# Optimization experiments

Hardware: AMD Instinct MI355X
Metric: run time of the kernel (lower is better)

The kernel has to match this reference:

```python
import jax, jax.numpy as jnp
import numpy as np

NQ = 4          # n_qubits -> 2**4 = 16 amplitudes
NL = 3          # n_layers
TWO_PI = 2.0 * np.pi
BN_EPS = 1e-5


def _ry_batched(t):
    # t: [B] -> [B,2,2] complex64
    c, s = jnp.cos(t / 2), jnp.sin(t / 2)
    g = jnp.stack([jnp.stack([c, -s], -1), jnp.stack([s, c], -1)], -2)
    return g.astype(jnp.complex64)


def _ry(t):
    c, s = jnp.cos(t / 2), jnp.sin(t / 2)
    return jnp.stack([jnp.stack([c, -s]), jnp.stack([s, c])]).astype(jnp.complex64)


def _rz(t):
    e = jnp.stack([jnp.exp(-0.5j * t), jnp.exp(0.5j * t)]).astype(jnp.complex64)
    return jnp.diag(e)


def _apply_1q(state, gate, wire, batched):
    # state: [B,2,2,2,2]; gate: [2,2] or [B,2,2]
    s = jnp.moveaxis(state, wire + 1, -1)
    if batched:
        s = jnp.einsum('bij,b...j->b...i', gate, s)
    else:
        s = jnp.einsum('ij,...j->...i', gate, s)
    return jnp.moveaxis(s, -1, wire + 1)


def _apply_cnot(state, c, t):
    s = jnp.moveaxis(state, (c + 1, t + 1), (-2, -1))
    s = jnp.stack([s[..., 0, :], s[..., 1, ::-1]], axis=-2)  # flip target when control=1
    return jnp.moveaxis(s, (-2, -1), (c + 1, t + 1))


def _circuit(angles, weights):
    # angles: [B, NQ] float32; weights: [NL, NQ, 2]
    B = angles.shape[0]
    state = jnp.zeros((B,) + (2,) * NQ, jnp.complex64)
    state = state.at[(slice(None),) + (0,) * NQ].set(1.0)
    # input encoding RYs (per-sample angles -> batched gates)
    for i in range(NQ):
        state = _apply_1q(state, _ry_batched(angles[:, i]), i, True)
    for layer in range(NL):
        for i in range(NQ):
            state = _apply_1q(state, _ry(weights[layer, i, 0]), i, False)
            state = _apply_1q(state, _rz(weights[layer, i, 1]), i, False)
        for i in range(NQ - 1):
            state = _apply_cnot(state, i, i + 1)
        state = _apply_cnot(state, NQ - 1, 0)
    probs = jnp.abs(state) ** 2  # [B,2,2,2,2] real
    zs = []
    for i in range(NQ):
        axes = tuple(a for a in range(1, NQ + 1) if a != i + 1)
        pm = probs.sum(axis=axes)  # [B,2]
        zs.append(pm[:, 0] - pm[:, 1])
    return jnp.stack(zs, -1).astype(jnp.float32)  # [B,NQ]


def setup_inputs() -> dict:
    key = jax.random.key(0)
    ks = jax.random.split(key, 4)
    B = 524288
    x = jax.random.normal(ks[0], (B, 16), jnp.float32)
    weights = jax.random.normal(ks[1], (NL, NQ, 2), jnp.float32)
    fc_w = jax.random.normal(ks[2], (4, NQ), jnp.float32) / np.sqrt(NQ)
    fc_b = jax.random.normal(ks[3], (4,), jnp.float32) * 0.01
    gamma = jnp.ones((4,), jnp.float32)
    beta = jnp.zeros((4,), jnp.float32)
    return {"x": x, "weights": weights, "fc_w": fc_w, "fc_b": fc_b,
            "gamma": gamma, "beta": beta}


def reference(x, weights, fc_w, fc_b, gamma, beta):
    inp = x.reshape(x.shape[0], -1)[:, :NQ]
    mn, mx = inp.min(), inp.max()  # global min/max as in the torch code
    angles = TWO_PI * (inp - mn) / (mx - mn + 1e-8)
    q = _circuit(angles, weights)                # [B,4] PauliZ expvals
    out = q @ fc_w.T + fc_b                      # Linear(4,4)
    mean = out.mean(0)
    var = out.var(0)                             # biased, as torch BN training
    return gamma * (out - mean) / jnp.sqrt(var + BN_EPS) + beta
```

## Files before the change

### kernel.cpp

```cpp
#include <hip/hip_runtime.h>
#include <math.h>

#define TWO_PI_F 6.28318530717958647692f
#define BN_EPS_F 1e-5f

#define MINK_OFF 0
#define MAXK_OFF 16
#define STAT_OFF 32
#define STAT_STRIDE 32
#define A_OFF 288
#define UR_OFF 384
#define UI_OFF 640

__device__ __forceinline__ unsigned f2key(float f) {
  unsigned u = __float_as_uint(f);
  return (u & 0x80000000u) ? ~u : (u | 0x80000000u);
}
__device__ __forceinline__ float key2f(unsigned k) {
  unsigned u = (k & 0x80000000u) ? (k ^ 0x80000000u) : ~k;
  return __uint_as_float(u);
}

__global__ void k_init(const float* __restrict__ w, const float* __restrict__ fc_w,
                       float* __restrict__ wsf) {
  int t = threadIdx.x;
  if (t == 0) {
    unsigned* wsu = (unsigned*)wsf;
    wsu[MINK_OFF] = 0xFFFFFFFFu;
    wsu[MAXK_OFF] = 0x00000000u;
#pragma unroll
    for (int j = 0; j < 8; ++j) wsf[STAT_OFF + j * STAT_STRIDE] = 0.0f;
    for (int j = 0; j < 4; ++j)
      for (int k = 0; k < 16; ++k) {
        float s = 0.f;
        for (int i = 0; i < 4; ++i)
          s += fc_w[j * 4 + i] * ((k & (8 >> i)) ? -1.f : 1.f);
        wsf[A_OFF + j * 16 + k] = s;
      }
  }
  if (t < 16) {
    float sr[16], si[16];
#pragma unroll
    for (int k = 0; k < 16; ++k) { sr[k] = (k == t) ? 1.f : 0.f; si[k] = 0.f; }
#pragma unroll
    for (int l = 0; l < 3; ++l) {
#pragma unroll
      for (int i = 0; i < 4; ++i) {
        const int m = 8 >> i;
        float ryc, rys, rzc, rzs;
        __sincosf(0.5f * w[(l * 4 + i) * 2 + 0], &rys, &ryc);
        __sincosf(0.5f * w[(l * 4 + i) * 2 + 1], &rzs, &rzc);
#pragma unroll
        for (int k = 0; k < 16; ++k) {
          if (!(k & m)) {
            int k1 = k | m;
            float a0r = sr[k], a0i = si[k], a1r = sr[k1], a1i = si[k1];
            sr[k]  = ryc * a0r - rys * a1r;
            si[k]  = ryc * a0i - rys * a1i;
            sr[k1] = rys * a0r + ryc * a1r;
            si[k1] = rys * a0i + ryc * a1i;
          }
        }
#pragma unroll
        for (int k = 0; k < 16; ++k) {
          float ps = (k & m) ? rzs : -rzs;
          float r = sr[k], ii = si[k];
          sr[k] = r * rzc - ii * ps;
          si[k] = r * ps + ii * rzc;
        }
      }
#pragma unroll
      for (int c = 0; c < 4; ++c) {
        const int mc = 8 >> c;
        const int mt = 8 >> ((c + 1) & 3);
#pragma unroll
        for (int k = 0; k < 16; ++k) {
          if ((k & mc) && !(k & mt)) {
            int k2 = k | mt;
            float tt;
            tt = sr[k]; sr[k] = sr[k2]; sr[k2] = tt;
            tt = si[k]; si[k] = si[k2]; si[k2] = tt;
          }
        }
      }
    }
#pragma unroll
    for (int k = 0; k < 16; ++k) {
      wsf[UR_OFF + k * 16 + t] = sr[k];
      wsf[UI_OFF + k * 16 + t] = si[k];
    }
  }
}

__global__ __launch_bounds__(256) void k_minmax(const float* __restrict__ x,
                                                unsigned* __restrict__ wsu, int B) {
  float fmn = __builtin_inff();
  float fmx = -__builtin_inff();
  for (int r = blockIdx.x * blockDim.x + threadIdx.x; r < B;
       r += gridDim.x * blockDim.x) {
    float4 v = *(const float4*)(x + (size_t)r * 16);
    fmn = fminf(fmn, fminf(fminf(v.x, v.y), fminf(v.z, v.w)));
    fmx = fmaxf(fmx, fmaxf(fmaxf(v.x, v.y), fmaxf(v.z, v.w)));
  }
#pragma unroll
  for (int d = 32; d; d >>= 1) {
    fmn = fminf(fmn, __shfl_down(fmn, d));
    fmx = fmaxf(fmx, __shfl_down(fmx, d));
  }
  __shared__ float smn[4], smx[4];
  int wave = threadIdx.x >> 6, lane = threadIdx.x & 63;
  if (lane == 0) { smn[wave] = fmn; smx[wave] = fmx; }
  __syncthreads();
  if (threadIdx.x == 0) {
    float bmn = fminf(fminf(smn[0], smn[1]), fminf(smn[2], smn[3]));
    float bmx = fmaxf(fmaxf(smx[0], smx[1]), fmaxf(smx[2], smx[3]));
    atomicMin(&wsu[MINK_OFF], f2key(bmn));
    atomicMax(&wsu[MAXK_OFF], f2key(bmx));
  }
}

__global__ __launch_bounds__(256) void k_main(const float* __restrict__ x,
                                              const float* __restrict__ wsf,
                                              const float* __restrict__ fc_b,
                                              float* __restrict__ out, int B) {
  int b = blockIdx.x * 256 + threadIdx.x;
  const unsigned* wsu = (const unsigned*)wsf;
  float mn = key2f(wsu[MINK_OFF]);
  float mx = key2f(wsu[MAXK_OFF]);
  float denom = mx - mn + 1e-8f;

  float o[4] = {0.f, 0.f, 0.f, 0.f};
  if (b < B) {
    float4 xv = *(const float4*)(x + (size_t)b * 16);
    float ang[4] = {TWO_PI_F * (xv.x - mn) / denom, TWO_PI_F * (xv.y - mn) / denom,
                    TWO_PI_F * (xv.z - mn) / denom, TWO_PI_F * (xv.w - mn) / denom};
    float cq[4], sq[4];
#pragma unroll
    for (int i = 0; i < 4; ++i) __sincosf(0.5f * ang[i], &sq[i], &cq[i]);

    float v[16];
#pragma unroll
    for (int k = 0; k < 16; ++k) {
      v[k] = ((k & 8) ? sq[0] : cq[0]) * ((k & 4) ? sq[1] : cq[1]) *
             ((k & 2) ? sq[2] : cq[2]) * ((k & 1) ? sq[3] : cq[3]);
    }

    const float* __restrict__ Ur = wsf + UR_OFF;
    const float* __restrict__ Ui = wsf + UI_OFF;
    float yr[16], yi[16];
#pragma unroll
    for (int k = 0; k < 16; ++k) { yr[k] = 0.f; yi[k] = 0.f; }
#pragma unroll
    for (int a = 0; a < 16; ++a) {
      float va = v[a];
#pragma unroll
      for (int k = 0; k < 16; ++k) {
        yr[k] = fmaf(Ur[k * 16 + a], va, yr[k]);
        yi[k] = fmaf(Ui[k * 16 + a], va, yi[k]);
      }
    }

    const float* __restrict__ A = wsf + A_OFF;
    o[0] = fc_b[0]; o[1] = fc_b[1]; o[2] = fc_b[2]; o[3] = fc_b[3];
#pragma unroll
    for (int k = 0; k < 16; ++k) {
      float p = yr[k] * yr[k] + yi[k] * yi[k];
      o[0] = fmaf(A[0 * 16 + k], p, o[0]);
      o[1] = fmaf(A[1 * 16 + k], p, o[1]);
      o[2] = fmaf(A[2 * 16 + k], p, o[2]);
      o[3] = fmaf(A[3 * 16 + k], p, o[3]);
    }
    *(float4*)(out + (size_t)b * 4) = make_float4(o[0], o[1], o[2], o[3]);
  }

  float vals[8] = {o[0], o[1], o[2], o[3],
                   o[0] * o[0], o[1] * o[1], o[2] * o[2], o[3] * o[3]};
#pragma unroll
  for (int j = 0; j < 8; ++j) {
#pragma unroll
    for (int d = 32; d; d >>= 1) vals[j] += __shfl_down(vals[j], d);
  }
  __shared__ float red[4][8];
  int wave = threadIdx.x >> 6, lane = threadIdx.x & 63;
  if (lane == 0) {
#pragma unroll
    for (int j = 0; j < 8; ++j) red[wave][j] = vals[j];
  }
  __syncthreads();
  if (threadIdx.x < 8) {
    float s = red[0][threadIdx.x] + red[1][threadIdx.x] + red[2][threadIdx.x] +
              red[3][threadIdx.x];
    atomicAdd((float*)wsf + STAT_OFF + threadIdx.x * STAT_STRIDE, s);
  }
}

__global__ __launch_bounds__(256) void k_final(float* __restrict__ out,
                                               const float* __restrict__ wsf,
                                               const float* __restrict__ gamma,
                                               const float* __restrict__ beta, int B) {
  int b = blockIdx.x * 256 + threadIdx.x;
  if (b >= B) return;
  float inv = 1.0f / (float)B;
  float4 v = *(float4*)(out + (size_t)b * 4);
  float vv[4] = {v.x, v.y, v.z, v.w};
  float res[4];
#pragma unroll
  for (int j = 0; j < 4; ++j) {
    float mean = wsf[STAT_OFF + j * STAT_STRIDE] * inv;
    float var = wsf[STAT_OFF + (4 + j) * STAT_STRIDE] * inv - mean * mean;
    res[j] = gamma[j] * (vv[j] - mean) * rsqrtf(var + BN_EPS_F) + beta[j];
  }
  *(float4*)(out + (size_t)b * 4) = make_float4(res[0], res[1], res[2], res[3]);
}

extern "C" void kernel_launch(void* const* d_in, const int* in_sizes, int n_in,
                              void* d_out, int out_size, void* d_ws, size_t ws_size,
                              hipStream_t stream) {
  const float* x     = (const float*)d_in[0];
  const float* w     = (const float*)d_in[1];
  const float* fc_w  = (const float*)d_in[2];
  const float* fc_b  = (const float*)d_in[3];
  const float* gamma = (const float*)d_in[4];
  const float* beta  = (const float*)d_in[5];
  float* out = (float*)d_out;
  float* wsf = (float*)d_ws;
  unsigned* wsu = (unsigned*)d_ws;
  int B = in_sizes[0] / 16;

  k_init<<<1, 64, 0, stream>>>(w, fc_w, wsf);
  k_minmax<<<1024, 256, 0, stream>>>(x, wsu, B);
  k_main<<<(B + 255) / 256, 256, 0, stream>>>(x, wsf, fc_b, out, B);
  k_final<<<(B + 255) / 256, 256, 0, stream>>>(out, wsf, gamma, beta, B);
}
```

Measured before the change: 137.6 us.

## Fuse minmax, circuit, and batchnorm into one cooperative grid-synced kernel

Replaces the four-kernel pipeline with a single cooperative kernel. Each thread loads its four samples once and keeps them in registers across two grid syncs: one for the global min/max, one for the batch-norm statistics. This removes the separate min/max pass over the input, the write and re-read of the intermediate output, and several launches. It also processes two samples per inner loop to reuse table loads and drops the bias, which cancels under batch norm. It relies on every block being co-resident, and it keeps a multi-kernel fallback if the cooperative launch fails.

```diff
diff --git a/kernel.cpp b/kernel.cpp
--- a/kernel.cpp
+++ b/kernel.cpp
@@ -1,16 +1,21 @@
 #include <hip/hip_runtime.h>
+#include <hip/hip_cooperative_groups.h>
 #include <math.h>
+
+namespace cg = cooperative_groups;
 
 #define TWO_PI_F 6.28318530717958647692f
 #define BN_EPS_F 1e-5f
-
-#define MINK_OFF 0
-#define MAXK_OFF 16
-#define STAT_OFF 32
+#define NBC 512
+#define NT 256
+
+#define STAT_OFF 0
 #define STAT_STRIDE 32
-#define A_OFF 288
-#define UR_OFF 384
-#define UI_OFF 640
+#define BMIN_OFF 256
+#define BMAX_OFF 768
+#define TAB_OFF 1280
+#define MINK_OFF 1856
+#define MAXK_OFF 1888
 
 __device__ __forceinline__ unsigned f2key(float f) {
   unsigned u = __float_as_uint(f);
@@ -21,27 +26,13 @@
   return __uint_as_float(u);
 }
 
-__global__ void k_init(const float* __restrict__ w, const float* __restrict__ fc_w,
-                       float* __restrict__ wsf) {
-  int t = threadIdx.x;
-  if (t == 0) {
-    unsigned* wsu = (unsigned*)wsf;
-    wsu[MINK_OFF] = 0xFFFFFFFFu;
-    wsu[MAXK_OFF] = 0x00000000u;
-#pragma unroll
-    for (int j = 0; j < 8; ++j) wsf[STAT_OFF + j * STAT_STRIDE] = 0.0f;
-    for (int j = 0; j < 4; ++j)
-      for (int k = 0; k < 16; ++k) {
-        float s = 0.f;
-        for (int i = 0; i < 4; ++i)
-          s += fc_w[j * 4 + i] * ((k & (8 >> i)) ? -1.f : 1.f);
-        wsf[A_OFF + j * 16 + k] = s;
-      }
-  }
-  if (t < 16) {
+__device__ void build_tables(int tid, const float* __restrict__ w,
+                             const float* __restrict__ fc_w, float* wsf,
+                             bool init_keys) {
+  if (tid < 16) {
     float sr[16], si[16];
 #pragma unroll
-    for (int k = 0; k < 16; ++k) { sr[k] = (k == t) ? 1.f : 0.f; si[k] = 0.f; }
+    for (int k = 0; k < 16; ++k) { sr[k] = (k == tid) ? 1.f : 0.f; si[k] = 0.f; }
 #pragma unroll
     for (int l = 0; l < 3; ++l) {
 #pragma unroll
@@ -55,8 +46,8 @@
           if (!(k & m)) {
             int k1 = k | m;
             float a0r = sr[k], a0i = si[k], a1r = sr[k1], a1i = si[k1];
-            sr[k]  = ryc * a0r - rys * a1r;
-            si[k]  = ryc * a0i - rys * a1i;
+            sr[k] = ryc * a0r - rys * a1r;
+            si[k] = ryc * a0i - rys * a1i;
             sr[k1] = rys * a0r + ryc * a1r;
             si[k1] = rys * a0i + ryc * a1i;
           }
@@ -86,16 +77,208 @@
     }
 #pragma unroll
     for (int k = 0; k < 16; ++k) {
-      wsf[UR_OFF + k * 16 + t] = sr[k];
-      wsf[UI_OFF + k * 16 + t] = si[k];
-    }
-  }
-}
-
-__global__ __launch_bounds__(256) void k_minmax(const float* __restrict__ x,
-                                                unsigned* __restrict__ wsu, int B) {
-  float fmn = __builtin_inff();
-  float fmx = -__builtin_inff();
+      wsf[TAB_OFF + tid * 16 + k] = sr[k];
+      wsf[TAB_OFF + 256 + tid * 16 + k] = si[k];
+    }
+  } else if (tid == 16) {
+    for (int k = 0; k < 16; ++k)
+      for (int j = 0; j < 4; ++j) {
+        float s = 0.f;
+        for (int i = 0; i < 4; ++i)
+          s += fc_w[j * 4 + i] * ((k & (8 >> i)) ? -1.f : 1.f);
+        wsf[TAB_OFF + 512 + k * 4 + j] = s;
+      }
+  } else if (tid == 17 && init_keys) {
+    unsigned* wsu = (unsigned*)wsf;
+    wsu[MINK_OFF] = 0xFFFFFFFFu;
+    wsu[MAXK_OFF] = 0x00000000u;
+  } else if (tid >= 24 && tid < 32) {
+    wsf[STAT_OFF + (tid - 24) * STAT_STRIDE] = 0.0f;
+  }
+}
+
+template <int PAIR>
+__device__ __forceinline__ void qfc_pair(const float* __restrict__ tab,
+                                         const float* c0, const float* s0,
+                                         const float* c1, const float* s1,
+                                         float* o0, float* o1) {
+  const float* __restrict__ Ur = tab;
+  const float* __restrict__ Ui = tab + 256;
+  const float* __restrict__ At = tab + 512;
+  float A01_0[4] = {c0[0] * c0[1], c0[0] * s0[1], s0[0] * c0[1], s0[0] * s0[1]};
+  float A23_0[4] = {c0[2] * c0[3], c0[2] * s0[3], s0[2] * c0[3], s0[2] * s0[3]};
+  float A01_1[4] = {c1[0] * c1[1], c1[0] * s1[1], s1[0] * c1[1], s1[0] * s1[1]};
+  float A23_1[4] = {c1[2] * c1[3], c1[2] * s1[3], s1[2] * c1[3], s1[2] * s1[3]};
+  float yr0[16], yi0[16], yr1[16], yi1[16];
+#pragma unroll
+  for (int k = 0; k < 16; ++k) { yr0[k] = yi0[k] = yr1[k] = yi1[k] = 0.f; }
+#pragma unroll
+  for (int a = 0; a < 16; ++a) {
+    float va0 = A01_0[a >> 2] * A23_0[a & 3];
+    float va1 = A01_1[a >> 2] * A23_1[a & 3];
+#pragma unroll
+    for (int k = 0; k < 16; ++k) {
+      float ur = Ur[a * 16 + k], ui = Ui[a * 16 + k];
+      yr0[k] = fmaf(ur, va0, yr0[k]);
+      yi0[k] = fmaf(ui, va0, yi0[k]);
+      yr1[k] = fmaf(ur, va1, yr1[k]);
+      yi1[k] = fmaf(ui, va1, yi1[k]);
+    }
+  }
+#pragma unroll
+  for (int j = 0; j < 4; ++j) { o0[j] = 0.f; o1[j] = 0.f; }
+#pragma unroll
+  for (int k = 0; k < 16; ++k) {
+    float p0 = fmaf(yr0[k], yr0[k], yi0[k] * yi0[k]);
+    float p1 = fmaf(yr1[k], yr1[k], yi1[k] * yi1[k]);
+#pragma unroll
+    for (int j = 0; j < 4; ++j) {
+      float av = At[k * 4 + j];
+      o0[j] = fmaf(av, p0, o0[j]);
+      o1[j] = fmaf(av, p1, o1[j]);
+    }
+  }
+}
+
+__global__ __launch_bounds__(NT, 2) void k_fused(
+    const float* __restrict__ x, const float* __restrict__ w,
+    const float* __restrict__ fc_w, const float* __restrict__ gamma,
+    const float* __restrict__ beta, float* wsf,
+    const float* __restrict__ tab, float* __restrict__ out, int B) {
+  cg::grid_group grid = cg::this_grid();
+  const int tid = threadIdx.x;
+  const int gtid = blockIdx.x * NT + tid;
+  const int H = NBC * NT;
+  const int wv = tid >> 6, ln = tid & 63;
+  __shared__ float sred[4][8];
+
+  float4 xs[4];
+  bool hp[4];
+#pragma unroll
+  for (int p = 0; p < 4; ++p) {
+    int s = gtid + p * H;
+    hp[p] = s < B;
+    xs[p] = hp[p] ? *(const float4*)(x + (size_t)s * 16) : make_float4(0, 0, 0, 0);
+  }
+  float fmn = __builtin_inff(), fmx = -__builtin_inff();
+#pragma unroll
+  for (int p = 0; p < 4; ++p) {
+    if (hp[p]) {
+      fmn = fminf(fmn, fminf(fminf(xs[p].x, xs[p].y), fminf(xs[p].z, xs[p].w)));
+      fmx = fmaxf(fmx, fmaxf(fmaxf(xs[p].x, xs[p].y), fmaxf(xs[p].z, xs[p].w)));
+    }
+  }
+#pragma unroll
+  for (int d = 32; d; d >>= 1) {
+    fmn = fminf(fmn, __shfl_down(fmn, d));
+    fmx = fmaxf(fmx, __shfl_down(fmx, d));
+  }
+  if (ln == 0) { sred[wv][0] = fmn; sred[wv][1] = fmx; }
+  __syncthreads();
+  if (tid == 0) {
+    wsf[BMIN_OFF + blockIdx.x] =
+        fminf(fminf(sred[0][0], sred[1][0]), fminf(sred[2][0], sred[3][0]));
+    wsf[BMAX_OFF + blockIdx.x] =
+        fmaxf(fmaxf(sred[0][1], sred[1][1]), fmaxf(sred[2][1], sred[3][1]));
+  }
+  if (blockIdx.x == 0) build_tables(tid, w, fc_w, wsf, false);
+
+  __threadfence();
+  grid.sync();
+
+  float gm = __builtin_inff(), gM = -__builtin_inff();
+#pragma unroll
+  for (int q = 0; q < NBC / 64; ++q) {
+    int i = ln + q * 64;
+    gm = fminf(gm, wsf[BMIN_OFF + i]);
+    gM = fmaxf(gM, wsf[BMAX_OFF + i]);
+  }
+#pragma unroll
+  for (int d = 32; d; d >>= 1) {
+    gm = fminf(gm, __shfl_down(gm, d));
+    gM = fmaxf(gM, __shfl_down(gM, d));
+  }
+  gm = __shfl(gm, 0);
+  gM = __shfl(gM, 0);
+  const float ssc = TWO_PI_F * 0.5f / (gM - gm + 1e-8f);
+
+  float o[4][4];
+#pragma unroll
+  for (int pp = 0; pp < 2; ++pp) {
+    const float4 xa = xs[pp * 2], xb = xs[pp * 2 + 1];
+    float a0[4] = {xa.x, xa.y, xa.z, xa.w};
+    float a1[4] = {xb.x, xb.y, xb.z, xb.w};
+    float c0[4], s0[4], c1[4], s1[4];
+#pragma unroll
+    for (int i = 0; i < 4; ++i) {
+      __sincosf((a0[i] - gm) * ssc, &s0[i], &c0[i]);
+      __sincosf((a1[i] - gm) * ssc, &s1[i], &c1[i]);
+    }
+    qfc_pair<0>(tab, c0, s0, c1, s1, o[pp * 2], o[pp * 2 + 1]);
+  }
+
+  float vals[8];
+#pragma unroll
+  for (int j = 0; j < 4; ++j) {
+    float s = 0.f, ss = 0.f;
+#pragma unroll
+    for (int p = 0; p < 4; ++p) {
+      float v = hp[p] ? o[p][j] : 0.f;
+      s += v;
+      ss = fmaf(v, v, ss);
+    }
+    vals[j] = s;
+    vals[4 + j] = ss;
+  }
+#pragma unroll
+  for (int j = 0; j < 8; ++j) {
+#pragma unroll
+    for (int d = 32; d; d >>= 1) vals[j] += __shfl_down(vals[j], d);
+  }
+  __syncthreads();
+  if (ln == 0) {
+#pragma unroll
+    for (int j = 0; j < 8; ++j) sred[wv][j] = vals[j];
+  }
+  __syncthreads();
+  if (tid < 8) {
+    float s = sred[0][tid] + sred[1][tid] + sred[2][tid] + sred[3][tid];
+    atomicAdd(wsf + STAT_OFF + tid * STAT_STRIDE, s);
+  }
+
+  __threadfence();
+  grid.sync();
+
+  const float inv = 1.0f / (float)B;
+  float sc[4], sh[4];
+#pragma unroll
+  for (int j = 0; j < 4; ++j) {
+    float mean = wsf[STAT_OFF + j * STAT_STRIDE] * inv;
+    float var = wsf[STAT_OFF + (4 + j) * STAT_STRIDE] * inv - mean * mean;
+    float is = rsqrtf(var + BN_EPS_F);
+    sc[j] = gamma[j] * is;
+    sh[j] = beta[j] - mean * sc[j];
+  }
+#pragma unroll
+  for (int p = 0; p < 4; ++p) {
+    if (hp[p]) {
+      int s = gtid + p * H;
+      *(float4*)(out + (size_t)s * 4) =
+          make_float4(fmaf(o[p][0], sc[0], sh[0]), fmaf(o[p][1], sc[1], sh[1]),
+                      fmaf(o[p][2], sc[2], sh[2]), fmaf(o[p][3], sc[3], sh[3]));
+    }
+  }
+}
+
+__global__ void k_init_fb(const float* __restrict__ w,
+                          const float* __restrict__ fc_w, float* wsf) {
+  build_tables(threadIdx.x, w, fc_w, wsf, true);
+}
+
+__global__ __launch_bounds__(256) void k_minmax_fb(const float* __restrict__ x,
+                                                   unsigned* __restrict__ wsu,
+                                                   int B) {
+  float fmn = __builtin_inff(), fmx = -__builtin_inff();
   for (int r = blockIdx.x * blockDim.x + threadIdx.x; r < B;
        r += gridDim.x * blockDim.x) {
     float4 v = *(const float4*)(x + (size_t)r * 16);
@@ -108,96 +291,62 @@
     fmx = fmaxf(fmx, __shfl_down(fmx, d));
   }
   __shared__ float smn[4], smx[4];
-  int wave = threadIdx.x >> 6, lane = threadIdx.x & 63;
-  if (lane == 0) { smn[wave] = fmn; smx[wave] = fmx; }
+  int wv = threadIdx.x >> 6, ln = threadIdx.x & 63;
+  if (ln == 0) { smn[wv] = fmn; smx[wv] = fmx; }
   __syncthreads();
   if (threadIdx.x == 0) {
-    float bmn = fminf(fminf(smn[0], smn[1]), fminf(smn[2], smn[3]));
-    float bmx = fmaxf(fmaxf(smx[0], smx[1]), fmaxf(smx[2], smx[3]));
-    atomicMin(&wsu[MINK_OFF], f2key(bmn));
-    atomicMax(&wsu[MAXK_OFF], f2key(bmx));
-  }
-}
-
-__global__ __launch_bounds__(256) void k_main(const float* __restrict__ x,
-                                              const float* __restrict__ wsf,
-                                              const float* __restrict__ fc_b,
-                                              float* __restrict__ out, int B) {
+    atomicMin(&wsu[MINK_OFF],
+              f2key(fminf(fminf(smn[0], smn[1]), fminf(smn[2], smn[3]))));
+    atomicMax(&wsu[MAXK_OFF],
+              f2key(fmaxf(fmaxf(smx[0], smx[1]), fmaxf(smx[2], smx[3]))));
+  }
+}
+
+__global__ __launch_bounds__(256) void k_main_fb(const float* __restrict__ x,
+                                                 float* wsf,
+                                                 const float* __restrict__ tab,
+                                                 float* __restrict__ out, int B) {
   int b = blockIdx.x * 256 + threadIdx.x;
   const unsigned* wsu = (const unsigned*)wsf;
   float mn = key2f(wsu[MINK_OFF]);
   float mx = key2f(wsu[MAXK_OFF]);
-  float denom = mx - mn + 1e-8f;
-
-  float o[4] = {0.f, 0.f, 0.f, 0.f};
+  const float ssc = TWO_PI_F * 0.5f / (mx - mn + 1e-8f);
+  float o0[4] = {0, 0, 0, 0}, o1[4];
   if (b < B) {
     float4 xv = *(const float4*)(x + (size_t)b * 16);
-    float ang[4] = {TWO_PI_F * (xv.x - mn) / denom, TWO_PI_F * (xv.y - mn) / denom,
-                    TWO_PI_F * (xv.z - mn) / denom, TWO_PI_F * (xv.w - mn) / denom};
-    float cq[4], sq[4];
-#pragma unroll
-    for (int i = 0; i < 4; ++i) __sincosf(0.5f * ang[i], &sq[i], &cq[i]);
-
-    float v[16];
-#pragma unroll
-    for (int k = 0; k < 16; ++k) {
-      v[k] = ((k & 8) ? sq[0] : cq[0]) * ((k & 4) ? sq[1] : cq[1]) *
-             ((k & 2) ? sq[2] : cq[2]) * ((k & 1) ? sq[3] : cq[3]);
-    }
-
-    const float* __restrict__ Ur = wsf + UR_OFF;
-    const float* __restrict__ Ui = wsf + UI_OFF;
-    float yr[16], yi[16];
-#pragma unroll
-    for (int k = 0; k < 16; ++k) { yr[k] = 0.f; yi[k] = 0.f; }
-#pragma unroll
-    for (int a = 0; a < 16; ++a) {
-      float va = v[a];
-#pragma unroll
-      for (int k = 0; k < 16; ++k) {
-        yr[k] = fmaf(Ur[k * 16 + a], va, yr[k]);
-        yi[k] = fmaf(Ui[k * 16 + a], va, yi[k]);
-      }
-    }
-
-    const float* __restrict__ A = wsf + A_OFF;
-    o[0] = fc_b[0]; o[1] = fc_b[1]; o[2] = fc_b[2]; o[3] = fc_b[3];
-#pragma unroll
-    for (int k = 0; k < 16; ++k) {
-      float p = yr[k] * yr[k] + yi[k] * yi[k];
-      o[0] = fmaf(A[0 * 16 + k], p, o[0]);
-      o[1] = fmaf(A[1 * 16 + k], p, o[1]);
-      o[2] = fmaf(A[2 * 16 + k], p, o[2]);
-      o[3] = fmaf(A[3 * 16 + k], p, o[3]);
-    }
-    *(float4*)(out + (size_t)b * 4) = make_float4(o[0], o[1], o[2], o[3]);
-  }
-
-  float vals[8] = {o[0], o[1], o[2], o[3],
-                   o[0] * o[0], o[1] * o[1], o[2] * o[2], o[3] * o[3]};
+    float a0[4] = {xv.x, xv.y, xv.z, xv.w};
+    float c0[4], s0[4];
+#pragma unroll
+    for (int i = 0; i < 4; ++i) __sincosf((a0[i] - mn) * ssc, &s0[i], &c0[i]);
+    qfc_pair<1>(tab, c0, s0, c0, s0, o0, o1);
+    *(float4*)(out + (size_t)b * 4) = make_float4(o0[0], o0[1], o0[2], o0[3]);
+  }
+  float vals[8] = {o0[0], o0[1], o0[2], o0[3],
+                   o0[0] * o0[0], o0[1] * o0[1], o0[2] * o0[2], o0[3] * o0[3]};
 #pragma unroll
   for (int j = 0; j < 8; ++j) {
 #pragma unroll
     for (int d = 32; d; d >>= 1) vals[j] += __shfl_down(vals[j], d);
   }
   __shared__ float red[4][8];
-  int wave = threadIdx.x >> 6, lane = threadIdx.x & 63;
-  if (lane == 0) {
-#pragma unroll
-    for (int j = 0; j < 8; ++j) red[wave][j] = vals[j];
+  int wv = threadIdx.x >> 6, ln = threadIdx.x & 63;
+  if (ln == 0) {
+#pragma unroll
+    for (int j = 0; j < 8; ++j) red[wv][j] = vals[j];
   }
   __syncthreads();
   if (threadIdx.x < 8) {
     float s = red[0][threadIdx.x] + red[1][threadIdx.x] + red[2][threadIdx.x] +
               red[3][threadIdx.x];
-    atomicAdd((float*)wsf + STAT_OFF + threadIdx.x * STAT_STRIDE, s);
-  }
-}
-
-__global__ __launch_bounds__(256) void k_final(float* __restrict__ out,
-                                               const float* __restrict__ wsf,
-                                               const float* __restrict__ gamma,
-                                               const float* __restrict__ beta, int B) {
+    atomicAdd(wsf + STAT_OFF + threadIdx.x * STAT_STRIDE, s);
+  }
+}
+
+__global__ __launch_bounds__(256) void k_final_fb(float* __restrict__ out,
+                                                  const float* __restrict__ wsf,
+                                                  const float* __restrict__ gamma,
+                                                  const float* __restrict__ beta,
+                                                  int B) {
   int b = blockIdx.x * 256 + threadIdx.x;
   if (b >= B) return;
   float inv = 1.0f / (float)B;
@@ -216,19 +365,25 @@
 extern "C" void kernel_launch(void* const* d_in, const int* in_sizes, int n_in,
                               void* d_out, int out_size, void* d_ws, size_t ws_size,
                               hipStream_t stream) {
-  const float* x     = (const float*)d_in[0];
-  const float* w     = (const float*)d_in[1];
-  const float* fc_w  = (const float*)d_in[2];
-  const float* fc_b  = (const float*)d_in[3];
+  const float* x = (const float*)d_in[0];
+  const float* w = (const float*)d_in[1];
+  const float* fc_w = (const float*)d_in[2];
   const float* gamma = (const float*)d_in[4];
-  const float* beta  = (const float*)d_in[5];
+  const float* beta = (const float*)d_in[5];
   float* out = (float*)d_out;
   float* wsf = (float*)d_ws;
-  unsigned* wsu = (unsigned*)d_ws;
+  const float* tab = wsf + TAB_OFF;
   int B = in_sizes[0] / 16;
 
-  k_init<<<1, 64, 0, stream>>>(w, fc_w, wsf);
-  k_minmax<<<1024, 256, 0, stream>>>(x, wsu, B);
-  k_main<<<(B + 255) / 256, 256, 0, stream>>>(x, wsf, fc_b, out, B);
-  k_final<<<(B + 255) / 256, 256, 0, stream>>>(out, wsf, gamma, beta, B);
-}
+  void* args[] = {(void*)&x,    (void*)&w,   (void*)&fc_w,
+                  (void*)&gamma, (void*)&beta, (void*)&wsf,
+                  (void*)&tab,  (void*)&out, (void*)&B};
+  hipError_t e = hipLaunchCooperativeKernel((void*)k_fused, dim3(NBC), dim3(NT),
+                                            args, 0, stream);
+  if (e != hipSuccess) {
+    k_init_fb<<<1, 64, 0, stream>>>(w, fc_w, wsf);
+    k_minmax_fb<<<1024, 256, 0, stream>>>(x, (unsigned*)d_ws, B);
+    k_main_fb<<<(B + 255) / 256, 256, 0, stream>>>(x, wsf, tab, out, B);
+    k_final_fb<<<(B + 255) / 256, 256, 0, stream>>>(out, wsf, gamma, beta, B);
+  }
+}
```

Measured after the change: 295.9 us. 2.15x slower.
